# Performance work log

Measured on AMD Instinct MI355X. Metric: run time of the kernel, lower is better.

## Reference

```python
import jax, jax.numpy as jnp
import numpy as np
import math

EMBED_DIM = 1024
NUM_HEADS = 16
D_K = EMBED_DIM // NUM_HEADS
B, S = 2, 2048


def setup_inputs() -> dict:
    key = jax.random.key(0)
    ks = jax.random.split(key, 6)
    scale = 1.0 / math.sqrt(EMBED_DIM)
    x = jax.random.normal(ks[0], (B, S, EMBED_DIM), dtype=jnp.float32)
    mask = jax.random.randint(ks[1], (B, S), 0, 2) > 0  # True = masked-out key
    wq = jax.random.normal(ks[2], (EMBED_DIM, EMBED_DIM), dtype=jnp.float32) * scale
    wk = jax.random.normal(ks[3], (EMBED_DIM, EMBED_DIM), dtype=jnp.float32) * scale
    wv = jax.random.normal(ks[4], (EMBED_DIM, EMBED_DIM), dtype=jnp.float32) * scale
    wo = jax.random.normal(ks[5], (EMBED_DIM, EMBED_DIM), dtype=jnp.float32) * scale
    return {"x": x, "mask": mask, "wq": wq, "wk": wk, "wv": wv, "wo": wo}


def reference(x, mask, wq, wk, wv, wo):
    b, s, _ = x.shape
    # torch nn.Linear(bias=False): y = x @ W.T
    q = (x @ wq.T).reshape(b, s, NUM_HEADS, D_K).transpose(0, 2, 1, 3)  # [B,H,S,Dk]
    k = (x @ wk.T).reshape(b, s, NUM_HEADS, D_K).transpose(0, 2, 1, 3)
    v = (x @ wv.T).reshape(b, s, NUM_HEADS, D_K).transpose(0, 2, 1, 3)
    scores = jnp.einsum('bhqd,bhkd->bhqk', q, k) / math.sqrt(D_K)
    # mask [B,S] -> [B,1,1,S]: key-padding mask, True filled with -1e9
    scores = jnp.where(mask[:, None, None, :], jnp.float32(-1e9), scores)
    attn = jax.nn.softmax(scores, axis=-1)
    # dropout in eval mode -> identity
    out = jnp.einsum('bhqk,bhkd->bhqd', attn, v)
    out = out.transpose(0, 2, 1, 3).reshape(b, s, EMBED_DIM)
    return out @ wo.T
```

## Files before the change

### kernel.cpp

```cpp
#include <hip/hip_runtime.h>
#include <hip/hip_bf16.h>


typedef unsigned short u16;
typedef unsigned int u32;
using short8 = __attribute__((ext_vector_type(8))) short;
using f32x4  = __attribute__((ext_vector_type(4))) float;

#define WS_XB    0u
#define WS_WQKV  8388608u
#define WS_WOB   14680064u
#define WS_QB    16777216u
#define WS_KB    25165824u
#define WS_VTB   33554432u
#define WS_OB    41943040u

__device__ __forceinline__ u16 f2bf(float f) {
  u32 u = __float_as_uint(f);
  u += 0x7fffu + ((u >> 16) & 1u);
  return (u16)(u >> 16);
}

__device__ __forceinline__ ushort4 pk4(f32x4 v) {
  ushort4 r; r.x = f2bf(v[0]); r.y = f2bf(v[1]); r.z = f2bf(v[2]); r.w = f2bf(v[3]);
  return r;
}

__device__ __forceinline__ u32 pkbf2(float lo, float hi) {
  union { __hip_bfloat162 b; u32 u; } c;
  c.b = __float22bfloat162_rn(make_float2(lo, hi));
  return c.u;
}

__device__ __forceinline__ void gload16(const void* g, void* l) {
  __builtin_amdgcn_global_load_lds(
      (const __attribute__((address_space(1))) u32*)g,
      (__attribute__((address_space(3))) u32*)l, 16, 0, 0);
}

#define KSCALE 0.18033688011112042f

__global__ void convert_k(const float* __restrict__ x, const float* __restrict__ wq,
                          const float* __restrict__ wk, const float* __restrict__ wv,
                          const float* __restrict__ wo,
                          u16* __restrict__ xb, u16* __restrict__ wqkv, u16* __restrict__ wob) {
  size_t g = ((size_t)blockIdx.x * 256 + threadIdx.x) * 4;
  const float* s; u16* d;
  if (g < 4194304u)      { s = x  + g;            d = xb   + g; }
  else if (g < 5242880u) { s = wq + (g - 4194304u); d = wqkv + (g - 4194304u); }
  else if (g < 6291456u) { s = wk + (g - 5242880u); d = wqkv + 1048576u + (g - 5242880u); }
  else if (g < 7340032u) { s = wv + (g - 6291456u); d = wqkv + 2097152u + (g - 6291456u); }
  else                   { s = wo + (g - 7340032u); d = wob  + (g - 7340032u); }
  float4 v = *(const float4*)s;
  f32x4 vv = {v.x, v.y, v.z, v.w};
  *(ushort4*)d = pk4(vv);
}

__global__ void gemm_qkv(const u16* __restrict__ A, const u16* __restrict__ Bt,
                         u16* __restrict__ qb, u16* __restrict__ kb, u16* __restrict__ vtb) {
  __shared__ __align__(16) u16 As[128 * 64];
  __shared__ __align__(16) u16 Bs[128 * 64];
  const int tid  = threadIdx.x;
  const int wave = tid >> 6, lane = tid & 63;
  const int c16  = lane & 15, quad = lane >> 4;
  const int tile_m = blockIdx.x * 128;
  const int tile_n = blockIdx.y * 128;
  const int wm = (wave >> 1) * 64, wn = (wave & 1) * 64;
  const int srow = wave * 32 + (lane >> 3);
  const int sc   = lane & 7;
  const int which = blockIdx.y >> 3;
  const bool swp  = (which < 2);

  const u16* Pa = swp ? Bs : As;
  const u16* Pb = swp ? As : Bs;
  const int  ra = swp ? wn : wm;
  const int  rb = swp ? wm : wn;

  f32x4 acc[4][4] = {};

  for (int k0 = 0; k0 < 1024; k0 += 64) {
    __syncthreads();
#pragma unroll
    for (int j = 0; j < 4; ++j) {
      int row = srow + j * 8;
      int cp  = sc ^ (row & 7);
      gload16(A  + (size_t)(tile_m + row) * 1024 + k0 + cp * 8, As + row * 64 + sc * 8);
      gload16(Bt + (size_t)(tile_n + row) * 1024 + k0 + cp * 8, Bs + row * 64 + sc * 8);
    }
    __syncthreads();
#pragma unroll
    for (int kc = 0; kc < 2; ++kc) {
      const int ch = ((kc * 4 + quad) ^ (c16 & 7)) * 8;
      short8 fa[4], fb[4];
#pragma unroll
      for (int i = 0; i < 4; ++i)
        fa[i] = *(const short8*)(Pa + (ra + i * 16 + c16) * 64 + ch);
#pragma unroll
      for (int j = 0; j < 4; ++j)
        fb[j] = *(const short8*)(Pb + (rb + j * 16 + c16) * 64 + ch);
#pragma unroll
      for (int i = 0; i < 4; ++i)
#pragma unroll
        for (int j = 0; j < 4; ++j)
          acc[i][j] = __builtin_amdgcn_mfma_f32_16x16x32_bf16(fa[i], fb[j], acc[i][j], 0, 0, 0);
    }
  }

  if (which == 2) {
#pragma unroll
    for (int i = 0; i < 4; ++i) {
      int m0 = tile_m + wm + i * 16 + quad * 4;
      int bb = m0 >> 11, ss0 = m0 & 2047;
#pragma unroll
      for (int j = 0; j < 4; ++j) {
        int f = (tile_n & 1023) + wn + j * 16 + c16;
        int h = f >> 6, d = f & 63;
        *(ushort4*)(vtb + ((size_t)(bb * 16 + h) * 64 + d) * 2048 + ss0) = pk4(acc[i][j]);
      }
    }
  } else {
    u16* dstb = which ? kb : qb;
#pragma unroll
    for (int i = 0; i < 4; ++i) {
      int full = (tile_n & 1023) + wn + i * 16 + quad * 4;
      int h = full >> 6, d0 = full & 63;
#pragma unroll
      for (int j = 0; j < 4; ++j) {
        int t = tile_m + wm + j * 16 + c16;
        int bb = t >> 11, ss = t & 2047;
        f32x4 v = acc[i][j];
        if (which == 0) { v[0] *= KSCALE; v[1] *= KSCALE; v[2] *= KSCALE; v[3] *= KSCALE; }
        *(ushort4*)(dstb + ((size_t)(bb * 16 + h) * 2048 + ss) * 64 + d0) = pk4(v);
      }
    }
  }
}

__global__ __launch_bounds__(256) void attn_k(const u16* __restrict__ qb, const u16* __restrict__ kb,
                                              const u16* __restrict__ vtb, const int* __restrict__ mask,
                                              u16* __restrict__ ob) {
  __shared__ __align__(16) u16 Ks[2][64 * 64];
  __shared__ __align__(16) u16 Vs[2][64 * 64];
  __shared__ __align__(16) u16 Ps[128 * 64];
  __shared__ u32 mask2[1024];

  const int tid  = threadIdx.x;
  const int wave = tid >> 6, lane = tid & 63;
  const int c16  = lane & 15, g4 = lane >> 4;
  const int bh   = blockIdx.y;
  const int bidx = bh >> 4, h = bh & 15;
  const int q0   = blockIdx.x * 128;

  {
    int4 m0 = *(const int4*)(mask + bidx * 2048 + tid * 8);
    int4 m1 = *(const int4*)(mask + bidx * 2048 + tid * 8 + 4);
    uint4 dd;
    dd.x = (m0.x ? 0u : 0xFFFFu) | (m0.y ? 0u : 0xFFFF0000u);
    dd.y = (m0.z ? 0u : 0xFFFFu) | (m0.w ? 0u : 0xFFFF0000u);
    dd.z = (m1.x ? 0u : 0xFFFFu) | (m1.y ? 0u : 0xFFFF0000u);
    dd.w = (m1.z ? 0u : 0xFFFFu) | (m1.w ? 0u : 0xFFFF0000u);
    *(uint4*)(mask2 + tid * 4) = dd;
  }

  const u16* qg = qb + ((size_t)bh * 2048 + q0 + wave * 32) * 64;
  short8 qf[2][2];
#pragma unroll
  for (int kc = 0; kc < 2; ++kc)
#pragma unroll
    for (int nj = 0; nj < 2; ++nj)
      qf[kc][nj] = *(const short8*)(qg + (nj * 16 + c16) * 64 + kc * 32 + g4 * 8);

  const u16* kg = kb  + (size_t)bh * 2048 * 64;
  const u16* vg = vtb + (size_t)bh * 64 * 2048;
  {
#pragma unroll
    for (int j = 0; j < 2; ++j) {
      int r  = j * 32 + (tid >> 3);
      int cp = (tid & 7) ^ (r & 7);
      gload16(kg + (size_t)r * 64 + cp * 8,   &Ks[0][j * 2048 + tid * 8]);
      gload16(vg + (size_t)r * 2048 + cp * 8, &Vs[0][j * 2048 + tid * 8]);
    }
  }
  __syncthreads();

  short8 ones;
#pragma unroll
  for (int i = 0; i < 8; ++i) ones[i] = (short)0x3F80;

  f32x4 O[2][4] = {};
  f32x4 L[2] = {};

#pragma unroll 2
  for (int kt = 0; kt < 32; ++kt) {
    if (kt) __syncthreads();
    if (kt + 1 < 32) {
      const int nb = (kt + 1) & 1;
#pragma unroll
      for (int j = 0; j < 2; ++j) {
        int r  = j * 32 + (tid >> 3);
        int cp = (tid & 7) ^ (r & 7);
        gload16(kg + (size_t)((kt + 1) * 64 + r) * 64 + cp * 8, &Ks[nb][j * 2048 + tid * 8]);
        gload16(vg + (size_t)r * 2048 + (kt + 1) * 64 + cp * 8, &Vs[nb][j * 2048 + tid * 8]);
      }
    }
    const u16* ksb = Ks[kt & 1];
    const u16* vsb = Vs[kt & 1];

    f32x4 S[4][2] = {};
#pragma unroll
    for (int kc = 0; kc < 2; ++kc) {
      const int ch = ((kc * 4 + g4) ^ (c16 & 7)) * 8;
      short8 a[4];
#pragma unroll
      for (int mi = 0; mi < 4; ++mi)
        a[mi] = *(const short8*)(ksb + (mi * 16 + c16) * 64 + ch);
#pragma unroll
      for (int mi = 0; mi < 4; ++mi)
#pragma unroll
        for (int nj = 0; nj < 2; ++nj)
          S[mi][nj] = __builtin_amdgcn_mfma_f32_16x16x32_bf16(a[mi], qf[kc][nj], S[mi][nj], 0, 0, 0);
    }

    uint2 mk[4];
#pragma unroll
    for (int mi = 0; mi < 4; ++mi)
      mk[mi] = *(const uint2*)(mask2 + kt * 32 + mi * 8 + g4 * 2);

#pragma unroll
    for (int nj = 0; nj < 2; ++nj) {
      const int q = wave * 32 + nj * 16 + c16;
#pragma unroll
      for (int mi = 0; mi < 4; ++mi) {
        float p0 = __builtin_amdgcn_exp2f(S[mi][nj][0]);
        float p1 = __builtin_amdgcn_exp2f(S[mi][nj][1]);
        float p2 = __builtin_amdgcn_exp2f(S[mi][nj][2]);
        float p3 = __builtin_amdgcn_exp2f(S[mi][nj][3]);
        u32 lo = pkbf2(p0, p1) & mk[mi].x;
        u32 hi = pkbf2(p2, p3) & mk[mi].y;
        uint2 pkd; pkd.x = lo; pkd.y = hi;
        const int c = mi * 2 + (g4 >> 1);
        *(uint2*)(Ps + q * 64 + ((c ^ (c16 & 7)) * 8 + (g4 & 1) * 4)) = pkd;
      }
    }

#pragma unroll
    for (int kc = 0; kc < 2; ++kc) {
      const int ch = ((kc * 4 + g4) ^ (c16 & 7)) * 8;
      short8 a2[2], b2[4];
#pragma unroll
      for (int mi = 0; mi < 2; ++mi)
        a2[mi] = *(const short8*)(Ps + (wave * 32 + mi * 16 + c16) * 64 + ch);
#pragma unroll
      for (int nd = 0; nd < 4; ++nd)
        b2[nd] = *(const short8*)(vsb + (nd * 16 + c16) * 64 + ch);
#pragma unroll
      for (int mi = 0; mi < 2; ++mi) {
#pragma unroll
        for (int nd = 0; nd < 4; ++nd)
          O[mi][nd] = __builtin_amdgcn_mfma_f32_16x16x32_bf16(a2[mi], b2[nd], O[mi][nd], 0, 0, 0);
        L[mi] = __builtin_amdgcn_mfma_f32_16x16x32_bf16(a2[mi], ones, L[mi], 0, 0, 0);
      }
    }
  }

  u16* og = ob + ((size_t)(bidx * 2048 + q0 + wave * 32)) * 1024 + h * 64;
#pragma unroll
  for (int mi = 0; mi < 2; ++mi) {
    f32x4 linv;
#pragma unroll
    for (int r = 0; r < 4; ++r) linv[r] = 1.f / L[mi][r];
#pragma unroll
    for (int r = 0; r < 4; ++r) {
      int qrow = mi * 16 + g4 * 4 + r;
#pragma unroll
      for (int nd = 0; nd < 4; ++nd)
        og[(size_t)qrow * 1024 + nd * 16 + c16] = f2bf(O[mi][nd][r] * linv[r]);
    }
  }
}

__global__ __launch_bounds__(256) void gemm_out(const u16* __restrict__ A, const u16* __restrict__ Bt,
                         float* __restrict__ out) {
  __shared__ __align__(16) u16 As[128 * 64];
  __shared__ __align__(16) u16 Bs[64 * 64];
  const int tid  = threadIdx.x;
  const int wave = tid >> 6, lane = tid & 63;
  const int c16  = lane & 15, quad = lane >> 4;
  const int tile_m = blockIdx.x * 128;
  const int tile_n = blockIdx.y * 64;
  const int wm = wave * 32;
  const int sc   = lane & 7;

  f32x4 acc[4][2] = {};

  for (int k0 = 0; k0 < 1024; k0 += 64) {
    __syncthreads();
    {
      int rowa = tid >> 1;
      int sca  = (tid & 1) * 4 + (sc & 3);
    }
#pragma unroll
    for (int j = 0; j < 4; ++j) {
      int row = (tid >> 3) + j * 32;
      int cp  = sc ^ (row & 7);
      gload16(A + (size_t)(tile_m + row) * 1024 + k0 + cp * 8, As + row * 64 + sc * 8);
    }
#pragma unroll
    for (int j = 0; j < 2; ++j) {
      int row = (tid >> 3) + j * 32;
      int cp  = sc ^ (row & 7);
      gload16(Bt + (size_t)(tile_n + row) * 1024 + k0 + cp * 8, Bs + row * 64 + sc * 8);
    }
    __syncthreads();
#pragma unroll
    for (int kc = 0; kc < 2; ++kc) {
      const int ch = ((kc * 4 + quad) ^ (c16 & 7)) * 8;
      short8 fa[4], fb[2];
#pragma unroll
      for (int i = 0; i < 4; ++i)
        fa[i] = *(const short8*)(Bs + (i * 16 + c16) * 64 + ch);
#pragma unroll
      for (int j = 0; j < 2; ++j)
        fb[j] = *(const short8*)(As + (wm + j * 16 + c16) * 64 + ch);
#pragma unroll
      for (int i = 0; i < 4; ++i)
#pragma unroll
        for (int j = 0; j < 2; ++j)
          acc[i][j] = __builtin_amdgcn_mfma_f32_16x16x32_bf16(fa[i], fb[j], acc[i][j], 0, 0, 0);
    }
  }
#pragma unroll
  for (int i = 0; i < 4; ++i) {
    int f0 = tile_n + i * 16 + quad * 4;
#pragma unroll
    for (int j = 0; j < 2; ++j) {
      int t = tile_m + wm + j * 16 + c16;
      *(f32x4*)(out + (size_t)t * 1024 + f0) = acc[i][j];
    }
  }
}

extern "C" void kernel_launch(void* const* d_in, const int* in_sizes, int n_in,
                              void* d_out, int out_size, void* d_ws, size_t ws_size,
                              hipStream_t stream) {
  (void)in_sizes; (void)n_in; (void)out_size; (void)ws_size;
  const float* x    = (const float*)d_in[0];
  const int*   mask = (const int*)d_in[1];
  const float* wq   = (const float*)d_in[2];
  const float* wk   = (const float*)d_in[3];
  const float* wv   = (const float*)d_in[4];
  const float* wo   = (const float*)d_in[5];
  float* out = (float*)d_out;
  char*  ws  = (char*)d_ws;

  u16* xb   = (u16*)(ws + WS_XB);
  u16* wqkv = (u16*)(ws + WS_WQKV);
  u16* wob  = (u16*)(ws + WS_WOB);
  u16* qbuf = (u16*)(ws + WS_QB);
  u16* kbuf = (u16*)(ws + WS_KB);
  u16* vtb  = (u16*)(ws + WS_VTB);
  u16* obuf = (u16*)(ws + WS_OB);

  convert_k<<<8192, 256, 0, stream>>>(x, wq, wk, wv, wo, xb, wqkv, wob);
  gemm_qkv<<<dim3(32, 24), 256, 0, stream>>>(xb, wqkv, qbuf, kbuf, vtb);
  attn_k<<<dim3(16, 32), 256, 0, stream>>>(qbuf, kbuf, vtb, mask, obuf);
  gemm_out<<<dim3(32, 16), 256, 0, stream>>>(obuf, wob, out);
}
```

Before: 183.6 us.

## Prefetch K/V tiles through registers with single-buffered LDS in attention

After: 184.5 us. No clear change (+0.5%).

```diff
diff --git a/kernel.cpp b/kernel.cpp
--- a/kernel.cpp
+++ b/kernel.cpp
@@ -139,8 +139,8 @@
 __global__ __launch_bounds__(256) void attn_k(const u16* __restrict__ qb, const u16* __restrict__ kb,
                                               const u16* __restrict__ vtb, const int* __restrict__ mask,
                                               u16* __restrict__ ob) {
-  __shared__ __align__(16) u16 Ks[2][64 * 64];
-  __shared__ __align__(16) u16 Vs[2][64 * 64];
+  __shared__ __align__(16) u16 Ks[64 * 64];
+  __shared__ __align__(16) u16 Vs[64 * 64];
   __shared__ __align__(16) u16 Ps[128 * 64];
   __shared__ u32 mask2[1024];
 
@@ -172,14 +172,23 @@
 
   const u16* kg = kb  + (size_t)bh * 2048 * 64;
   const u16* vg = vtb + (size_t)bh * 64 * 2048;
-  {
-#pragma unroll
-    for (int j = 0; j < 2; ++j) {
-      int r  = j * 32 + (tid >> 3);
-      int cp = (tid & 7) ^ (r & 7);
-      gload16(kg + (size_t)r * 64 + cp * 8,   &Ks[0][j * 2048 + tid * 8]);
-      gload16(vg + (size_t)r * 2048 + cp * 8, &Vs[0][j * 2048 + tid * 8]);
-    }
+
+  const int sr0 = tid >> 3;
+  const int sc  = tid & 7;
+
+  short8 kr[2], vr[2];
+#pragma unroll
+  for (int j = 0; j < 2; ++j) {
+    int r  = sr0 + j * 32;
+    int cp = sc ^ (r & 7);
+    kr[j] = *(const short8*)(kg + (size_t)r * 64 + cp * 8);
+    vr[j] = *(const short8*)(vg + (size_t)r * 2048 + cp * 8);
+  }
+#pragma unroll
+  for (int j = 0; j < 2; ++j) {
+    int r = sr0 + j * 32;
+    *(short8*)(Ks + r * 64 + sc * 8) = kr[j];
+    *(short8*)(Vs + r * 64 + sc * 8) = vr[j];
   }
   __syncthreads();
 
@@ -190,21 +199,17 @@
   f32x4 O[2][4] = {};
   f32x4 L[2] = {};
 
-#pragma unroll 2
+#pragma unroll 1
   for (int kt = 0; kt < 32; ++kt) {
-    if (kt) __syncthreads();
     if (kt + 1 < 32) {
-      const int nb = (kt + 1) & 1;
 #pragma unroll
       for (int j = 0; j < 2; ++j) {
-        int r  = j * 32 + (tid >> 3);
-        int cp = (tid & 7) ^ (r & 7);
-        gload16(kg + (size_t)((kt + 1) * 64 + r) * 64 + cp * 8, &Ks[nb][j * 2048 + tid * 8]);
-        gload16(vg + (size_t)r * 2048 + (kt + 1) * 64 + cp * 8, &Vs[nb][j * 2048 + tid * 8]);
-      }
-    }
-    const u16* ksb = Ks[kt & 1];
-    const u16* vsb = Vs[kt & 1];
+        int r  = sr0 + j * 32;
+        int cp = sc ^ (r & 7);
+        kr[j] = *(const short8*)(kg + (size_t)((kt + 1) * 64 + r) * 64 + cp * 8);
+        vr[j] = *(const short8*)(vg + (size_t)r * 2048 + (kt + 1) * 64 + cp * 8);
+      }
+    }
 
     f32x4 S[4][2] = {};
 #pragma unroll
@@ -213,7 +218,7 @@
       short8 a[4];
 #pragma unroll
       for (int mi = 0; mi < 4; ++mi)
-        a[mi] = *(const short8*)(ksb + (mi * 16 + c16) * 64 + ch);
+        a[mi] = *(const short8*)(Ks + (mi * 16 + c16) * 64 + ch);
 #pragma unroll
       for (int mi = 0; mi < 4; ++mi)
 #pragma unroll
@@ -252,7 +257,7 @@
         a2[mi] = *(const short8*)(Ps + (wave * 32 + mi * 16 + c16) * 64 + ch);
 #pragma unroll
       for (int nd = 0; nd < 4; ++nd)
-        b2[nd] = *(const short8*)(vsb + (nd * 16 + c16) * 64 + ch);
+        b2[nd] = *(const short8*)(Vs + (nd * 16 + c16) * 64 + ch);
 #pragma unroll
       for (int mi = 0; mi < 2; ++mi) {
 #pragma unroll
@@ -260,6 +265,17 @@
           O[mi][nd] = __builtin_amdgcn_mfma_f32_16x16x32_bf16(a2[mi], b2[nd], O[mi][nd], 0, 0, 0);
         L[mi] = __builtin_amdgcn_mfma_f32_16x16x32_bf16(a2[mi], ones, L[mi], 0, 0, 0);
       }
+    }
+
+    if (kt + 1 < 32) {
+      __syncthreads();
+#pragma unroll
+      for (int j = 0; j < 2; ++j) {
+        int r = sr0 + j * 32;
+        *(short8*)(Ks + r * 64 + sc * 8) = kr[j];
+        *(short8*)(Vs + r * 64 + sc * 8) = vr[j];
+      }
+      __syncthreads();
     }
   }
 
@@ -295,10 +311,6 @@
 
   for (int k0 = 0; k0 < 1024; k0 += 64) {
     __syncthreads();
-    {
-      int rowa = tid >> 1;
-      int sca  = (tid & 1) * 4 + (sc & 3);
-    }
 #pragma unroll
     for (int j = 0; j < 4; ++j) {
       int row = (tid >> 3) + j * 32;
```

## Load K/V fragments directly from global memory in attention, dropping LDS staging

Applied to the files above, without the earlier changes.

New measurement: 252.6 us. 1.38x slower.

```diff
diff --git a/kernel.cpp b/kernel.cpp
--- a/kernel.cpp
+++ b/kernel.cpp
@@ -136,11 +136,9 @@
   }
 }
 
-__global__ __launch_bounds__(256) void attn_k(const u16* __restrict__ qb, const u16* __restrict__ kb,
-                                              const u16* __restrict__ vtb, const int* __restrict__ mask,
-                                              u16* __restrict__ ob) {
-  __shared__ __align__(16) u16 Ks[2][64 * 64];
-  __shared__ __align__(16) u16 Vs[2][64 * 64];
+__global__ __launch_bounds__(256, 2) void attn_k(const u16* __restrict__ qb, const u16* __restrict__ kb,
+                                                 const u16* __restrict__ vtb, const int* __restrict__ mask,
+                                                 u16* __restrict__ ob) {
   __shared__ __align__(16) u16 Ps[128 * 64];
   __shared__ u32 mask2[1024];
 
@@ -170,17 +168,9 @@
     for (int nj = 0; nj < 2; ++nj)
       qf[kc][nj] = *(const short8*)(qg + (nj * 16 + c16) * 64 + kc * 32 + g4 * 8);
 
-  const u16* kg = kb  + (size_t)bh * 2048 * 64;
-  const u16* vg = vtb + (size_t)bh * 64 * 2048;
-  {
-#pragma unroll
-    for (int j = 0; j < 2; ++j) {
-      int r  = j * 32 + (tid >> 3);
-      int cp = (tid & 7) ^ (r & 7);
-      gload16(kg + (size_t)r * 64 + cp * 8,   &Ks[0][j * 2048 + tid * 8]);
-      gload16(vg + (size_t)r * 2048 + cp * 8, &Vs[0][j * 2048 + tid * 8]);
-    }
-  }
+  const u16* kB = kb  + (size_t)bh * 2048 * 64;
+  const u16* vB = vtb + (size_t)bh * 64 * 2048;
+
   __syncthreads();
 
   short8 ones;
@@ -190,36 +180,27 @@
   f32x4 O[2][4] = {};
   f32x4 L[2] = {};
 
-#pragma unroll 2
+#pragma unroll 1
   for (int kt = 0; kt < 32; ++kt) {
-    if (kt) __syncthreads();
-    if (kt + 1 < 32) {
-      const int nb = (kt + 1) & 1;
-#pragma unroll
-      for (int j = 0; j < 2; ++j) {
-        int r  = j * 32 + (tid >> 3);
-        int cp = (tid & 7) ^ (r & 7);
-        gload16(kg + (size_t)((kt + 1) * 64 + r) * 64 + cp * 8, &Ks[nb][j * 2048 + tid * 8]);
-        gload16(vg + (size_t)r * 2048 + (kt + 1) * 64 + cp * 8, &Vs[nb][j * 2048 + tid * 8]);
-      }
-    }
-    const u16* ksb = Ks[kt & 1];
-    const u16* vsb = Vs[kt & 1];
+    short8 ka[2][4], vb[2][4];
+#pragma unroll
+    for (int kc = 0; kc < 2; ++kc) {
+#pragma unroll
+      for (int mi = 0; mi < 4; ++mi)
+        ka[kc][mi] = *(const short8*)(kB + (size_t)(kt * 64 + mi * 16 + c16) * 64 + kc * 32 + g4 * 8);
+#pragma unroll
+      for (int nd = 0; nd < 4; ++nd)
+        vb[kc][nd] = *(const short8*)(vB + (size_t)(nd * 16 + c16) * 2048 + kt * 64 + kc * 32 + g4 * 8);
+    }
 
     f32x4 S[4][2] = {};
 #pragma unroll
-    for (int kc = 0; kc < 2; ++kc) {
-      const int ch = ((kc * 4 + g4) ^ (c16 & 7)) * 8;
-      short8 a[4];
+    for (int kc = 0; kc < 2; ++kc)
 #pragma unroll
       for (int mi = 0; mi < 4; ++mi)
-        a[mi] = *(const short8*)(ksb + (mi * 16 + c16) * 64 + ch);
-#pragma unroll
-      for (int mi = 0; mi < 4; ++mi)
 #pragma unroll
         for (int nj = 0; nj < 2; ++nj)
-          S[mi][nj] = __builtin_amdgcn_mfma_f32_16x16x32_bf16(a[mi], qf[kc][nj], S[mi][nj], 0, 0, 0);
-    }
+          S[mi][nj] = __builtin_amdgcn_mfma_f32_16x16x32_bf16(ka[kc][mi], qf[kc][nj], S[mi][nj], 0, 0, 0);
 
     uint2 mk[4];
 #pragma unroll
@@ -246,18 +227,15 @@
 #pragma unroll
     for (int kc = 0; kc < 2; ++kc) {
       const int ch = ((kc * 4 + g4) ^ (c16 & 7)) * 8;
-      short8 a2[2], b2[4];
+      short8 a2[2];
 #pragma unroll
       for (int mi = 0; mi < 2; ++mi)
         a2[mi] = *(const short8*)(Ps + (wave * 32 + mi * 16 + c16) * 64 + ch);
 #pragma unroll
-      for (int nd = 0; nd < 4; ++nd)
-        b2[nd] = *(const short8*)(vsb + (nd * 16 + c16) * 64 + ch);
-#pragma unroll
       for (int mi = 0; mi < 2; ++mi) {
 #pragma unroll
         for (int nd = 0; nd < 4; ++nd)
-          O[mi][nd] = __builtin_amdgcn_mfma_f32_16x16x32_bf16(a2[mi], b2[nd], O[mi][nd], 0, 0, 0);
+          O[mi][nd] = __builtin_amdgcn_mfma_f32_16x16x32_bf16(a2[mi], vb[kc][nd], O[mi][nd], 0, 0, 0);
         L[mi] = __builtin_amdgcn_mfma_f32_16x16x32_bf16(a2[mi], ones, L[mi], 0, 0, 0);
       }
     }
@@ -295,10 +273,6 @@
 
   for (int k0 = 0; k0 < 1024; k0 += 64) {
     __syncthreads();
-    {
-      int rowa = tid >> 1;
-      int sca  = (tid & 1) * 4 + (sc & 3);
-    }
 #pragma unroll
     for (int j = 0; j < 4; ++j) {
       int row = (tid >> 3) + j * 32;
```
